# Kernel tuning notes

Hardware: AMD Instinct MI355X
Metric: run time of the kernel (lower is better)

Reference implementation:

```python
import jax, jax.numpy as jnp
import numpy as np

N_HEAD = 16  # from init_kwargs

def setup_inputs() -> dict:
    key = jax.random.key(0)
    ks = jax.random.split(key, 10)
    B, T, C = 2, 2048, 1024
    s = 0.02
    x = jax.random.normal(ks[0], (B, T, C), dtype=jnp.float32)
    # Per-head q/k/v Linears (bias=False) concatenated along output dim -> [C, C]
    Wq = jax.random.normal(ks[1], (C, C), dtype=jnp.float32) * s
    Wk = jax.random.normal(ks[2], (C, C), dtype=jnp.float32) * s
    Wv = jax.random.normal(ks[3], (C, C), dtype=jnp.float32) * s
    Wproj = jax.random.normal(ks[4], (C, C), dtype=jnp.float32) * s
    bproj = jnp.zeros((C,), dtype=jnp.float32)
    W1 = jax.random.normal(ks[5], (C, 4 * C), dtype=jnp.float32) * s
    b1 = jnp.zeros((4 * C,), dtype=jnp.float32)
    W2 = jax.random.normal(ks[6], (4 * C, C), dtype=jnp.float32) * s
    b2 = jnp.zeros((C,), dtype=jnp.float32)
    return {"x": x, "Wq": Wq, "Wk": Wk, "Wv": Wv, "Wproj": Wproj,
            "bproj": bproj, "W1": W1, "b1": b1, "W2": W2, "b2": b2}


def reference(x, Wq, Wk, Wv, Wproj, bproj, W1, b1, W2, b2):
    B, T, C = x.shape
    H = N_HEAD
    hs = C // H
    # QKV projections, split into heads: [B, T, H, hs]
    q = (x @ Wq).reshape(B, T, H, hs)
    k = (x @ Wk).reshape(B, T, H, hs)
    v = (x @ Wv).reshape(B, T, H, hs)
    # NOTE: original scales by C**-0.5 where C = n_embd (full model dim)
    scale = jnp.asarray(C, x.dtype) ** -0.5
    scores = jnp.einsum('bqhd,bkhd->bhqk', q, k) * scale
    causal = jnp.tril(jnp.ones((T, T), dtype=bool))
    scores = jnp.where(causal, scores, -jnp.inf)
    wei = jax.nn.softmax(scores, axis=-1)
    attn = jnp.einsum('bhqk,bkhd->bqhd', wei, v).reshape(B, T, C)
    x = x + attn @ Wproj + bproj
    x = x + jax.nn.relu(x @ W1 + b1) @ W2 + b2
    return x
```

## Files before the change

### kernel.cpp

```cpp
#include <hip/hip_runtime.h>
#include <math.h>
#include <stdint.h>

#define B_  2
#define T_  2048
#define C_  1024
#define H_  16
#define HS_ 64
#define M_  4096

typedef unsigned short u16;
typedef u16   u16x4 __attribute__((ext_vector_type(4)));
typedef u16   u16x8 __attribute__((ext_vector_type(8)));
typedef float f32x4 __attribute__((ext_vector_type(4)));

typedef uint32_t __attribute__((address_space(1))) u32_as1;
typedef uint32_t __attribute__((address_space(3))) u32_as3;

__device__ __forceinline__ u16 f2bf(float f) {
    uint32_t u = __float_as_uint(f);
    u = (u + 0x7fffu + ((u >> 16) & 1u)) >> 16;
    return (u16)u;
}

__device__ __forceinline__ void gload_lds16(const void* g, void* l) {
    __builtin_amdgcn_global_load_lds((const u32_as1*)g, (u32_as3*)l, 16, 0, 0);
}

__device__ __forceinline__ f32x4 mfma_bf16(u16x8 a, u16x8 b, f32x4 c) {
    asm("v_mfma_f32_16x16x32_bf16 %0, %1, %2, %0" : "+v"(c) : "v"(a), "v"(b));
    return c;
}

__global__ __launch_bounds__(256)
void cast_f32_bf16(const float* __restrict__ x, u16* __restrict__ xb) {
    const int i = blockIdx.x * 256 + threadIdx.x;
    const float4* xi = (const float4*)x;
    float4 a = xi[2 * i], b = xi[2 * i + 1];
    u16x8 o;
    o[0] = f2bf(a.x); o[1] = f2bf(a.y); o[2] = f2bf(a.z); o[3] = f2bf(a.w);
    o[4] = f2bf(b.x); o[5] = f2bf(b.y); o[6] = f2bf(b.z); o[7] = f2bf(b.w);
    *(u16x8*)&xb[(size_t)i * 8] = o;
}

__global__ __launch_bounds__(256)
void transpose_cast(const float* __restrict__ W, u16* __restrict__ Wt, int K, int N) {
    __shared__ float tile[64][65];
    const int n0 = blockIdx.x * 64, k0 = blockIdx.y * 64;
    const int tid = threadIdx.x;
    #pragma unroll
    for (int p = 0; p < 16; ++p) {
        int idx = p * 256 + tid;
        int r = idx >> 6, c = idx & 63;
        tile[r][c] = W[(size_t)(k0 + r) * N + n0 + c];
    }
    __syncthreads();
    #pragma unroll
    for (int p = 0; p < 16; ++p) {
        int idx = p * 256 + tid;
        int r = idx >> 6, c = idx & 63;
        Wt[(size_t)(n0 + r) * K + k0 + c] = f2bf(tile[c][r]);
    }
}

__global__ __launch_bounds__(256)
void transpose4_cast(const float* __restrict__ A0, const float* __restrict__ A1,
                     const float* __restrict__ A2, const float* __restrict__ A3,
                     u16* __restrict__ Wt) {
    __shared__ float tile[64][65];
    const float* src = (blockIdx.z == 0) ? A0 : (blockIdx.z == 1) ? A1
                     : (blockIdx.z == 2) ? A2 : A3;
    u16* dst = Wt + (size_t)blockIdx.z * 1048576;
    const int n0 = blockIdx.x * 64, k0 = blockIdx.y * 64;
    const int tid = threadIdx.x;
    #pragma unroll
    for (int p = 0; p < 16; ++p) {
        int idx = p * 256 + tid;
        int r = idx >> 6, c = idx & 63;
        tile[r][c] = src[(size_t)(k0 + r) * 1024 + n0 + c];
    }
    __syncthreads();
    #pragma unroll
    for (int p = 0; p < 16; ++p) {
        int idx = p * 256 + tid;
        int r = idx >> 6, c = idx & 63;
        dst[(size_t)(n0 + r) * 1024 + k0 + c] = f2bf(tile[c][r]);
    }
}

enum { EP_QKV = 0, EP_PROJ = 1, EP_RELU = 2, EP_RESID = 3 };

template<int EP>
__global__ __launch_bounds__(256)
void gemm_bf16(const u16* __restrict__ A, const u16* __restrict__ Bt,
               const float* __restrict__ bias, const float* __restrict__ resid,
               float* __restrict__ fout, u16* __restrict__ bout,
               int N, int K) {
    __shared__ __align__(16) u16 Al[128 * 64];
    __shared__ __align__(16) u16 Bl[128 * 64];
    const int tid  = threadIdx.x;
    const int lane = tid & 63, w = tid >> 6;
    const int wr = w >> 1, wc = w & 1;
    const int brow = blockIdx.y * 128, bcol = blockIdx.x * 128;
    const int rg   = lane >> 3;
    const int csrc = (lane & 7) ^ rg;

    f32x4 acc[4][4];
    #pragma unroll
    for (int i = 0; i < 4; ++i)
        #pragma unroll
        for (int j = 0; j < 4; ++j)
            acc[i][j] = f32x4{0.f, 0.f, 0.f, 0.f};

    for (int k0 = 0; k0 < K; k0 += 64) {
        #pragma unroll
        for (int i = 0; i < 4; ++i) {
            const int seg = i * 4 + w;
            gload_lds16(A  + (size_t)(brow + seg * 8 + rg) * K + k0 + csrc * 8,
                        &Al[seg * 512]);
            gload_lds16(Bt + (size_t)(bcol + seg * 8 + rg) * K + k0 + csrc * 8,
                        &Bl[seg * 512]);
        }
        __syncthreads();
        #pragma unroll
        for (int kk = 0; kk < 2; ++kk) {
            u16x8 af[4], bfv[4];
            #pragma unroll
            for (int mi = 0; mi < 4; ++mi) {
                const int row = wr * 64 + mi * 16 + (lane & 15);
                const int ch  = (kk * 4 + (lane >> 4)) ^ (row & 7);
                af[mi] = *(const u16x8*)&Al[row * 64 + ch * 8];
            }
            #pragma unroll
            for (int nj = 0; nj < 4; ++nj) {
                const int row = wc * 64 + nj * 16 + (lane & 15);
                const int ch  = (kk * 4 + (lane >> 4)) ^ (row & 7);
                bfv[nj] = *(const u16x8*)&Bl[row * 64 + ch * 8];
            }
            #pragma unroll
            for (int mi = 0; mi < 4; ++mi)
                #pragma unroll
                for (int nj = 0; nj < 4; ++nj)
                    acc[mi][nj] = mfma_bf16(af[mi], bfv[nj], acc[mi][nj]);
        }
        __syncthreads();
    }

    const int g = lane >> 4, c16 = lane & 15;
    #pragma unroll
    for (int mi = 0; mi < 4; ++mi) {
        #pragma unroll
        for (int nj = 0; nj < 4; ++nj) {
            if (EP == EP_QKV) {
                const int col = bcol + wc * 64 + nj * 16 + c16;
                const int region = col >> 10, c = col & 1023;
                const int hh = c >> 6, d = c & 63;
                const int row0 = brow + wr * 64 + mi * 16 + g * 4;
                const int bb = row0 >> 11, t0 = row0 & 2047;
                if (region < 2) {
                    #pragma unroll
                    for (int r = 0; r < 4; ++r)
                        bout[(size_t)region * 4194304 +
                             (((size_t)(bb * 16 + hh)) * 2048 + t0 + r) * 64 + d] =
                            f2bf(acc[mi][nj][r]);
                } else {
                    u16x4 pk;
                    #pragma unroll
                    for (int r = 0; r < 4; ++r) pk[r] = f2bf(acc[mi][nj][r]);
                    *(u16x4*)&bout[(size_t)2 * 4194304 +
                                   (((size_t)(bb * 16 + hh)) * 64 + d) * 2048 + t0] = pk;
                }
            } else {
                #pragma unroll
                for (int r = 0; r < 4; ++r) {
                    const int row = brow + wr * 64 + mi * 16 + g * 4 + r;
                    const int col = bcol + wc * 64 + nj * 16 + c16;
                    const float vacc = acc[mi][nj][r];
                    if (EP == EP_PROJ) {
                        const float o = vacc + bias[col] + resid[(size_t)row * N + col];
                        fout[(size_t)row * N + col] = o;
                        bout[(size_t)row * N + col] = f2bf(o);
                    } else if (EP == EP_RELU) {
                        float o = vacc + bias[col];
                        o = fmaxf(o, 0.f);
                        bout[(size_t)row * N + col] = f2bf(o);
                    } else {
                        const float o = vacc + bias[col] + fout[(size_t)row * N + col];
                        fout[(size_t)row * N + col] = o;
                    }
                }
            }
        }
    }
}

__global__ __launch_bounds__(256)
void attn_mfma(const u16* __restrict__ q, const u16* __restrict__ k,
               const u16* __restrict__ vt, u16* __restrict__ o) {
    __shared__ __align__(16) u16 Kl[64 * 64];
    __shared__ __align__(16) u16 Vl[64 * 64];
    __shared__ __align__(16) u16 Pl[4 * 16 * 72];
    const int tid = threadIdx.x, lane = tid & 63, w = tid >> 6;
    const int g = lane >> 4, c16 = lane & 15;
    const int rg = lane >> 3, csrc = (lane & 7) ^ rg;
    const int pair = blockIdx.x, h = blockIdx.y, b = blockIdx.z;
    const float scale = 0.03125f;

    const size_t hb  = ((size_t)b * H_ + h) * T_ * HS_;
    const u16* qh = q  + hb;
    const u16* kh = k  + hb;
    const u16* vh = vt + hb;

    #pragma unroll
    for (int phase = 0; phase < 2; ++phase) {
        const int qt = phase ? (31 - pair) : pair;

        const size_t qrow_l = (size_t)(qt * 64 + w * 16 + c16);
        u16x8 qf[2];
        qf[0] = *(const u16x8*)&qh[qrow_l * 64 + g * 8];
        qf[1] = *(const u16x8*)&qh[qrow_l * 64 + 32 + g * 8];

        float m_run[4], l_run[4];
        f32x4 oacc[4];
        #pragma unroll
        for (int r = 0; r < 4; ++r) { m_run[r] = -INFINITY; l_run[r] = 0.f; }
        #pragma unroll
        for (int nt = 0; nt < 4; ++nt) oacc[nt] = f32x4{0.f, 0.f, 0.f, 0.f};

        for (int kv = 0; kv <= qt; ++kv) {
            __syncthreads();
            #pragma unroll
            for (int i = 0; i < 2; ++i) {
                const int seg = i * 4 + w;
                gload_lds16(kh + (size_t)(kv * 64 + seg * 8 + rg) * 64 + csrc * 8,
                            &Kl[seg * 512]);
                gload_lds16(vh + (size_t)(seg * 8 + rg) * T_ + kv * 64 + csrc * 8,
                            &Vl[seg * 512]);
            }
            __syncthreads();

            f32x4 s[4];
            #pragma unroll
            for (int kt = 0; kt < 4; ++kt) s[kt] = f32x4{0.f, 0.f, 0.f, 0.f};
            #pragma unroll
            for (int kt = 0; kt < 4; ++kt)
                #pragma unroll
                for (int kk = 0; kk < 2; ++kk) {
                    const int row = kt * 16 + c16;
                    const int ch  = (kk * 4 + g) ^ (row & 7);
                    u16x8 kf = *(const u16x8*)&Kl[row * 64 + ch * 8];
                    s[kt] = mfma_bf16(qf[kk], kf, s[kt]);
                }

            const bool last = (kv == qt);
            float sv[4][4];
            #pragma unroll
            for (int kt = 0; kt < 4; ++kt)
                #pragma unroll
                for (int r = 0; r < 4; ++r) {
                    float val = s[kt][r] * scale;
                    if (last && (kv * 64 + kt * 16 + c16) > (qt * 64 + w * 16 + g * 4 + r))
                        val = -INFINITY;
                    sv[kt][r] = val;
                }

            float pm[4];
            #pragma unroll
            for (int r = 0; r < 4; ++r)
                pm[r] = fmaxf(fmaxf(sv[0][r], sv[1][r]), fmaxf(sv[2][r], sv[3][r]));
            #pragma unroll
            for (int mask = 1; mask < 16; mask <<= 1)
                #pragma unroll
                for (int r = 0; r < 4; ++r)
                    pm[r] = fmaxf(pm[r], __shfl_xor(pm[r], mask));

            float corr[4];
            #pragma unroll
            for (int r = 0; r < 4; ++r) {
                const float nm = fmaxf(m_run[r], pm[r]);
                corr[r] = __expf(m_run[r] - nm);
                m_run[r] = nm;
            }

            float rs[4] = {0.f, 0.f, 0.f, 0.f};
            float ps[4][4];
            #pragma unroll
            for (int kt = 0; kt < 4; ++kt)
                #pragma unroll
                for (int r = 0; r < 4; ++r) {
                    const float p = __expf(sv[kt][r] - m_run[r]);
                    ps[kt][r] = p;
                    rs[r] += p;
                }
            #pragma unroll
            for (int mask = 1; mask < 16; mask <<= 1)
                #pragma unroll
                for (int r = 0; r < 4; ++r)
                    rs[r] += __shfl_xor(rs[r], mask);
            #pragma unroll
            for (int r = 0; r < 4; ++r) l_run[r] = l_run[r] * corr[r] + rs[r];
            #pragma unroll
            for (int nt = 0; nt < 4; ++nt)
                #pragma unroll
                for (int r = 0; r < 4; ++r) oacc[nt][r] *= corr[r];

            #pragma unroll
            for (int kt = 0; kt < 4; ++kt)
                #pragma unroll
                for (int r = 0; r < 4; ++r)
                    Pl[w * 1152 + (g * 4 + r) * 72 + kt * 16 + c16] = f2bf(ps[kt][r]);

            #pragma unroll
            for (int kkp = 0; kkp < 2; ++kkp) {
                u16x8 pf = *(const u16x8*)&Pl[w * 1152 + c16 * 72 + kkp * 32 + g * 8];
                #pragma unroll
                for (int nt = 0; nt < 4; ++nt) {
                    const int row = nt * 16 + c16;
                    const int ch  = (kkp * 4 + g) ^ (row & 7);
                    u16x8 vf = *(const u16x8*)&Vl[row * 64 + ch * 8];
                    oacc[nt] = mfma_bf16(pf, vf, oacc[nt]);
                }
            }
        }

        float inv[4];
        #pragma unroll
        for (int r = 0; r < 4; ++r) inv[r] = 1.f / l_run[r];
        const int orow = qt * 64 + w * 16;
        #pragma unroll
        for (int nt = 0; nt < 4; ++nt)
            #pragma unroll
            for (int r = 0; r < 4; ++r)
                o[((size_t)(b * T_ + orow + g * 4 + r)) * C_ + h * 64 + nt * 16 + c16] =
                    f2bf(oacc[nt][r] * inv[r]);
    }
}

extern "C" void kernel_launch(void* const* d_in, const int* in_sizes, int n_in,
                              void* d_out, int out_size, void* d_ws, size_t ws_size,
                              hipStream_t stream) {
    const float* x     = (const float*)d_in[0];
    const float* Wq    = (const float*)d_in[1];
    const float* Wk    = (const float*)d_in[2];
    const float* Wv    = (const float*)d_in[3];
    const float* Wproj = (const float*)d_in[4];
    const float* bproj = (const float*)d_in[5];
    const float* W1    = (const float*)d_in[6];
    const float* b1    = (const float*)d_in[7];
    const float* W2    = (const float*)d_in[8];
    const float* b2    = (const float*)d_in[9];
    float* out = (float*)d_out;

    u16* ws    = (u16*)d_ws;
    u16* Wqkvt = ws;
    u16* Wpt   = ws + 3145728;
    u16* W1t   = ws + 4194304;
    u16* W2t   = ws + 8388608;
    u16* xb    = ws + 12582912;
    u16* qb    = ws + 16777216;
    u16* ab    = ws + 29360128;
    u16* x1b   = xb;
    u16* h1b   = qb;

    dim3 blk(256);

    cast_f32_bf16<<<dim3(2048), blk, 0, stream>>>(x, xb);
    transpose4_cast<<<dim3(16, 16, 4), blk, 0, stream>>>(Wq, Wk, Wv, Wproj, Wqkvt);
    transpose_cast<<<dim3(64, 16), blk, 0, stream>>>(W1, W1t, 1024, 4096);
    transpose_cast<<<dim3(16, 64), blk, 0, stream>>>(W2, W2t, 4096, 1024);

    gemm_bf16<EP_QKV><<<dim3(24, 32), blk, 0, stream>>>(
        xb, Wqkvt, nullptr, nullptr, nullptr, qb, 3072, 1024);

    attn_mfma<<<dim3(16, 16, 2), blk, 0, stream>>>(
        qb, qb + 4194304, qb + 8388608, ab);

    gemm_bf16<EP_PROJ><<<dim3(8, 32), blk, 0, stream>>>(
        ab, Wpt, bproj, x, out, x1b, 1024, 1024);

    gemm_bf16<EP_RELU><<<dim3(32, 32), blk, 0, stream>>>(
        x1b, W1t, b1, nullptr, nullptr, h1b, 4096, 1024);

    gemm_bf16<EP_RESID><<<dim3(8, 32), blk, 0, stream>>>(
        h1b, W2t, b2, nullptr, out, nullptr, 1024, 4096);
}
```

Measured before the change: 358.1 us.

## Double-buffer LDS in attention and small GEMMs, remap attention blocks per XCD

Adds a DBUF template option to the GEMM. For the projection and FFN-down launches it prefetches the next K tile into a second LDS buffer while computing the current one, removing one barrier per iteration. The attention kernel likewise double-buffers K/V tiles and raises wave priority around the MFMA sections. It also switches to a 1D grid whose index is remapped so that blocks sharing a head land on the same XCD, aiming for better L2 reuse. The cost is doubled LDS use in those kernels, which may reduce occupancy.

```diff
diff --git a/kernel.cpp b/kernel.cpp
--- a/kernel.cpp
+++ b/kernel.cpp
@@ -90,14 +90,14 @@
 
 enum { EP_QKV = 0, EP_PROJ = 1, EP_RELU = 2, EP_RESID = 3 };
 
-template<int EP>
+template<int EP, bool DBUF>
 __global__ __launch_bounds__(256)
 void gemm_bf16(const u16* __restrict__ A, const u16* __restrict__ Bt,
                const float* __restrict__ bias, const float* __restrict__ resid,
                float* __restrict__ fout, u16* __restrict__ bout,
                int N, int K) {
-    __shared__ __align__(16) u16 Al[128 * 64];
-    __shared__ __align__(16) u16 Bl[128 * 64];
+    __shared__ __align__(16) u16 Al[(DBUF ? 2 : 1) * 128 * 64];
+    __shared__ __align__(16) u16 Bl[(DBUF ? 2 : 1) * 128 * 64];
     const int tid  = threadIdx.x;
     const int lane = tid & 63, w = tid >> 6;
     const int wr = w >> 1, wc = w & 1;
@@ -105,23 +105,36 @@
     const int rg   = lane >> 3;
     const int csrc = (lane & 7) ^ rg;
 
-    f32x4 acc[4][4];
-    #pragma unroll
-    for (int i = 0; i < 4; ++i)
-        #pragma unroll
-        for (int j = 0; j < 4; ++j)
-            acc[i][j] = f32x4{0.f, 0.f, 0.f, 0.f};
-
-    for (int k0 = 0; k0 < K; k0 += 64) {
+    auto stageg = [&](int k0, int buf) {
         #pragma unroll
         for (int i = 0; i < 4; ++i) {
             const int seg = i * 4 + w;
             gload_lds16(A  + (size_t)(brow + seg * 8 + rg) * K + k0 + csrc * 8,
-                        &Al[seg * 512]);
+                        &Al[buf * 8192 + seg * 512]);
             gload_lds16(Bt + (size_t)(bcol + seg * 8 + rg) * K + k0 + csrc * 8,
-                        &Bl[seg * 512]);
-        }
-        __syncthreads();
+                        &Bl[buf * 8192 + seg * 512]);
+        }
+    };
+
+    f32x4 acc[4][4];
+    #pragma unroll
+    for (int i = 0; i < 4; ++i)
+        #pragma unroll
+        for (int j = 0; j < 4; ++j)
+            acc[i][j] = f32x4{0.f, 0.f, 0.f, 0.f};
+
+    if (DBUF) stageg(0, 0);
+    int cur = 0;
+    for (int k0 = 0; k0 < K; k0 += 64) {
+        if (DBUF) {
+            __syncthreads();
+            if (k0 + 64 < K) stageg(k0 + 64, cur ^ 1);
+        } else {
+            stageg(k0, 0);
+            __syncthreads();
+        }
+        const u16* Ab = &Al[cur * 8192];
+        const u16* Bb = &Bl[cur * 8192];
         #pragma unroll
         for (int kk = 0; kk < 2; ++kk) {
             u16x8 af[4], bfv[4];
@@ -129,13 +142,13 @@
             for (int mi = 0; mi < 4; ++mi) {
                 const int row = wr * 64 + mi * 16 + (lane & 15);
                 const int ch  = (kk * 4 + (lane >> 4)) ^ (row & 7);
-                af[mi] = *(const u16x8*)&Al[row * 64 + ch * 8];
+                af[mi] = *(const u16x8*)&Ab[row * 64 + ch * 8];
             }
             #pragma unroll
             for (int nj = 0; nj < 4; ++nj) {
                 const int row = wc * 64 + nj * 16 + (lane & 15);
                 const int ch  = (kk * 4 + (lane >> 4)) ^ (row & 7);
-                bfv[nj] = *(const u16x8*)&Bl[row * 64 + ch * 8];
+                bfv[nj] = *(const u16x8*)&Bb[row * 64 + ch * 8];
             }
             #pragma unroll
             for (int mi = 0; mi < 4; ++mi)
@@ -143,7 +156,8 @@
                 for (int nj = 0; nj < 4; ++nj)
                     acc[mi][nj] = mfma_bf16(af[mi], bfv[nj], acc[mi][nj]);
         }
-        __syncthreads();
+        if (DBUF) cur ^= 1;
+        else __syncthreads();
     }
 
     const int g = lane >> 4, c16 = lane & 15;
@@ -197,13 +211,18 @@
 __global__ __launch_bounds__(256)
 void attn_mfma(const u16* __restrict__ q, const u16* __restrict__ k,
                const u16* __restrict__ vt, u16* __restrict__ o) {
-    __shared__ __align__(16) u16 Kl[64 * 64];
-    __shared__ __align__(16) u16 Vl[64 * 64];
+    __shared__ __align__(16) u16 Kl[2][64 * 64];
+    __shared__ __align__(16) u16 Vl[2][64 * 64];
     __shared__ __align__(16) u16 Pl[4 * 16 * 72];
     const int tid = threadIdx.x, lane = tid & 63, w = tid >> 6;
     const int g = lane >> 4, c16 = lane & 15;
     const int rg = lane >> 3, csrc = (lane & 7) ^ rg;
-    const int pair = blockIdx.x, h = blockIdx.y, b = blockIdx.z;
+
+    const int lin  = blockIdx.x;
+    const int xcd  = lin & 7, sub = lin >> 3;
+    const int grp  = xcd * 4 + (sub >> 4);
+    const int pair = sub & 15;
+    const int h = grp & 15, b = grp >> 4;
     const float scale = 0.03125f;
 
     const size_t hb  = ((size_t)b * H_ + h) * T_ * HS_;
@@ -211,6 +230,18 @@
     const u16* kh = k  + hb;
     const u16* vh = vt + hb;
 
+    auto stage = [&](int kv, int buf) {
+        #pragma unroll
+        for (int i = 0; i < 2; ++i) {
+            const int seg = i * 4 + w;
+            gload_lds16(kh + (size_t)(kv * 64 + seg * 8 + rg) * 64 + csrc * 8,
+                        &Kl[buf][seg * 512]);
+            gload_lds16(vh + (size_t)(seg * 8 + rg) * T_ + kv * 64 + csrc * 8,
+                        &Vl[buf][seg * 512]);
+        }
+    };
+
+    int cur = 0;
     #pragma unroll
     for (int phase = 0; phase < 2; ++phase) {
         const int qt = phase ? (31 - pair) : pair;
@@ -227,30 +258,27 @@
         #pragma unroll
         for (int nt = 0; nt < 4; ++nt) oacc[nt] = f32x4{0.f, 0.f, 0.f, 0.f};
 
+        __syncthreads();
+        stage(0, cur);
+
         for (int kv = 0; kv <= qt; ++kv) {
             __syncthreads();
-            #pragma unroll
-            for (int i = 0; i < 2; ++i) {
-                const int seg = i * 4 + w;
-                gload_lds16(kh + (size_t)(kv * 64 + seg * 8 + rg) * 64 + csrc * 8,
-                            &Kl[seg * 512]);
-                gload_lds16(vh + (size_t)(seg * 8 + rg) * T_ + kv * 64 + csrc * 8,
-                            &Vl[seg * 512]);
-            }
-            __syncthreads();
+            if (kv < qt) stage(kv + 1, cur ^ 1);
 
             f32x4 s[4];
             #pragma unroll
             for (int kt = 0; kt < 4; ++kt) s[kt] = f32x4{0.f, 0.f, 0.f, 0.f};
+            __builtin_amdgcn_s_setprio(1);
             #pragma unroll
             for (int kt = 0; kt < 4; ++kt)
                 #pragma unroll
                 for (int kk = 0; kk < 2; ++kk) {
                     const int row = kt * 16 + c16;
                     const int ch  = (kk * 4 + g) ^ (row & 7);
-                    u16x8 kf = *(const u16x8*)&Kl[row * 64 + ch * 8];
+                    u16x8 kf = *(const u16x8*)&Kl[cur][row * 64 + ch * 8];
                     s[kt] = mfma_bf16(qf[kk], kf, s[kt]);
                 }
+            __builtin_amdgcn_s_setprio(0);
 
             const bool last = (kv == qt);
             float sv[4][4];
@@ -310,6 +338,7 @@
                 for (int r = 0; r < 4; ++r)
                     Pl[w * 1152 + (g * 4 + r) * 72 + kt * 16 + c16] = f2bf(ps[kt][r]);
 
+            __builtin_amdgcn_s_setprio(1);
             #pragma unroll
             for (int kkp = 0; kkp < 2; ++kkp) {
                 u16x8 pf = *(const u16x8*)&Pl[w * 1152 + c16 * 72 + kkp * 32 + g * 8];
@@ -317,10 +346,12 @@
                 for (int nt = 0; nt < 4; ++nt) {
                     const int row = nt * 16 + c16;
                     const int ch  = (kkp * 4 + g) ^ (row & 7);
-                    u16x8 vf = *(const u16x8*)&Vl[row * 64 + ch * 8];
+                    u16x8 vf = *(const u16x8*)&Vl[cur][row * 64 + ch * 8];
                     oacc[nt] = mfma_bf16(pf, vf, oacc[nt]);
                 }
             }
+            __builtin_amdgcn_s_setprio(0);
+            cur ^= 1;
         }
 
         float inv[4];
@@ -369,18 +400,18 @@
     transpose_cast<<<dim3(64, 16), blk, 0, stream>>>(W1, W1t, 1024, 4096);
     transpose_cast<<<dim3(16, 64), blk, 0, stream>>>(W2, W2t, 4096, 1024);
 
-    gemm_bf16<EP_QKV><<<dim3(24, 32), blk, 0, stream>>>(
+    gemm_bf16<EP_QKV, false><<<dim3(24, 32), blk, 0, stream>>>(
         xb, Wqkvt, nullptr, nullptr, nullptr, qb, 3072, 1024);
 
-    attn_mfma<<<dim3(16, 16, 2), blk, 0, stream>>>(
+    attn_mfma<<<dim3(512), blk, 0, stream>>>(
         qb, qb + 4194304, qb + 8388608, ab);
 
-    gemm_bf16<EP_PROJ><<<dim3(8, 32), blk, 0, stream>>>(
+    gemm_bf16<EP_PROJ, true><<<dim3(8, 32), blk, 0, stream>>>(
         ab, Wpt, bproj, x, out, x1b, 1024, 1024);
 
-    gemm_bf16<EP_RELU><<<dim3(32, 32), blk, 0, stream>>>(
+    gemm_bf16<EP_RELU, false><<<dim3(32, 32), blk, 0, stream>>>(
         x1b, W1t, b1, nullptr, nullptr, h1b, 4096, 1024);
 
-    gemm_bf16<EP_RESID><<<dim3(8, 32), blk, 0, stream>>>(
+    gemm_bf16<EP_RESID, true><<<dim3(8, 32), blk, 0, stream>>>(
         h1b, W2t, b2, nullptr, out, nullptr, 1024, 4096);
 }
```

Result: no change. 363.3 us (+1.4%).
